# Optimization experiments

Hardware: AMD Instinct MI355X
Metric: run time of the kernel (lower is better)

The kernel has to match this reference:

```python
import jax, jax.numpy as jnp
import numpy as np

# Fully-refined octree (branching=2, initial_levels=7) == dense grid of resolution 128.
R = 128            # voxel grid resolution per axis (2**initial_levels)
SH_DIM = 9         # (sh_degree+1)**2, sh_degree=2
DATA_DIM = 28      # 3*SH_DIM + 1 (RGB SH coeffs + density)
N_STEPS = 128      # fixed ray-march step count (render_opt.n_steps)
BG = 1.0           # background brightness


def sh_basis(d):
    """Real SH basis up to degree 2 for unit directions d: [N,3] -> [N,9]."""
    x, y, z = d[:, 0], d[:, 1], d[:, 2]
    C0 = 0.28209479177387814
    C1 = 0.4886025119029199
    C2 = (1.0925484305920792, -1.0925484305920792, 0.31539156525252005,
          -1.0925484305920792, 0.5462742152960396)
    return jnp.stack([
        jnp.full_like(x, C0),
        -C1 * y, C1 * z, -C1 * x,
        C2[0] * x * y, C2[1] * y * z,
        C2[2] * (2.0 * z * z - x * x - y * y),
        C2[3] * x * z, C2[4] * (x * x - y * y),
    ], axis=-1)


def trilerp(grid, pts):
    """Trilinear interpolation. grid [R,R,R,C], pts [N,3] in grid coords."""
    Rg = grid.shape[0]
    p = jnp.clip(pts, 0.0, Rg - 1.0 - 1e-4)
    p0 = jnp.floor(p).astype(jnp.int32)
    w = p - p0.astype(p.dtype)
    out = jnp.zeros((pts.shape[0], grid.shape[-1]), grid.dtype)
    for dx in (0, 1):
        wx = w[:, 0] if dx else 1.0 - w[:, 0]
        for dy in (0, 1):
            wy = w[:, 1] if dy else 1.0 - w[:, 1]
            for dz in (0, 1):
                wz = w[:, 2] if dz else 1.0 - w[:, 2]
                out = out + (wx * wy * wz)[:, None] * grid[p0[:, 0] + dx, p0[:, 1] + dy, p0[:, 2] + dz]
    return out


def _render(grid, rays_o, rays_d, scaling, offset):
    dirs = rays_d / jnp.linalg.norm(rays_d, axis=-1, keepdims=True)   # world viewdirs
    o = rays_o * scaling + offset                                      # tree coords in [0,1]^3
    d = dirs * scaling
    delta_scale = 1.0 / jnp.linalg.norm(d, axis=-1)                    # world-space step scale
    invd = 1.0 / jnp.where(jnp.abs(d) > 1e-9, d, 1e-9)
    t1 = (0.0 - o) * invd
    t2 = (1.0 - o) * invd
    tmin = jnp.maximum(jnp.max(jnp.minimum(t1, t2), axis=-1), 0.0)
    tmax = jnp.min(jnp.maximum(t1, t2), axis=-1)
    valid = tmax > tmin
    dt = jnp.where(valid, (tmax - tmin) / N_STEPS, 0.0)                # per-ray step length
    basis = sh_basis(dirs)                                             # [N,9]
    N = rays_o.shape[0]

    def step(carry, i):
        T, rgb = carry
        t = tmin + (i.astype(grid.dtype) + 0.5) * dt
        pos = o + t[:, None] * d                                       # [N,3] in [0,1]^3
        vals = trilerp(grid, pos * R - 0.5)                            # [N,28]
        sigma = jnp.where(valid, jax.nn.relu(vals[:, -1]), 0.0)
        coeffs = vals[:, :3 * SH_DIM].reshape(N, 3, SH_DIM)
        c = jax.nn.sigmoid(jnp.einsum('nj,ncj->nc', basis, coeffs))    # [N,3]
        alpha = 1.0 - jnp.exp(-sigma * dt * delta_scale)
        rgb = rgb + (T * alpha)[:, None] * c
        T = T * (1.0 - alpha)
        return (T, rgb), None

    init = (jnp.ones((N,), grid.dtype), jnp.zeros((N, 3), grid.dtype))
    (T, rgb), _ = jax.lax.scan(step, init, jnp.arange(N_STEPS))
    return rgb + T[:, None] * BG


def setup_inputs() -> dict:
    key = jax.random.key(0)
    k1, k2, k3 = jax.random.split(key, 3)
    N = 32768
    rays_o = jax.random.uniform(k1, (N, 3), jnp.float32)               # inside unit cube
    rays_d = jax.random.normal(k2, (N, 3), jnp.float32)
    grid = jax.random.normal(k3, (R, R, R, DATA_DIM), jnp.float32) * 0.1  # octree leaf data
    scaling = jnp.ones((3,), jnp.float32)                              # 0.5/radius, radius=0.5
    offset = jnp.zeros((3,), jnp.float32)                              # 0.5 - center*scaling
    return {"rays_o": rays_o, "rays_d": rays_d, "grid": grid,
            "scaling": scaling, "offset": offset}


def reference(rays_o, rays_d, grid, scaling, offset):
    return _render(grid, rays_o, rays_d, scaling, offset)
```

## Files before the change

### kernel.cpp

```cpp
#include <hip/hip_runtime.h>
#include <math.h>

#define RGRID 128
#define NSTEPS 128
#define DATA_DIM 28

__device__ __forceinline__ float fast_rcp(float x) { return __builtin_amdgcn_rcpf(x); }

__global__ __launch_bounds__(256) void render_kernel(
    const float* __restrict__ rays_o,
    const float* __restrict__ rays_d,
    const float* __restrict__ grid,
    const float* __restrict__ scaling,
    const float* __restrict__ offset,
    float* __restrict__ out, int N)
{
    int tid = blockIdx.x * blockDim.x + threadIdx.x;
    int ray = tid >> 6;
    int lane = tid & 63;
    int s = lane >> 3;
    int c = lane & 7;
    if (ray >= N) return;

    float ox = rays_o[ray * 3 + 0], oy = rays_o[ray * 3 + 1], oz = rays_o[ray * 3 + 2];
    float rdx = rays_d[ray * 3 + 0], rdy = rays_d[ray * 3 + 1], rdz = rays_d[ray * 3 + 2];
    float sx = scaling[0], sy = scaling[1], sz = scaling[2];
    float fx = offset[0], fy = offset[1], fz = offset[2];

    float dn = rsqrtf(rdx * rdx + rdy * rdy + rdz * rdz);
    float dirx = rdx * dn, diry = rdy * dn, dirz = rdz * dn;

    float o0 = ox * sx + fx, o1 = oy * sy + fy, o2 = oz * sz + fz;
    float d0 = dirx * sx, d1 = diry * sy, d2 = dirz * sz;
    float delta_scale = rsqrtf(d0 * d0 + d1 * d1 + d2 * d2);

    float a0 = fabsf(d0) > 1e-9f ? d0 : 1e-9f;
    float a1 = fabsf(d1) > 1e-9f ? d1 : 1e-9f;
    float a2 = fabsf(d2) > 1e-9f ? d2 : 1e-9f;
    float i0 = 1.0f / a0, i1 = 1.0f / a1, i2 = 1.0f / a2;

    float t1x = (0.0f - o0) * i0, t2x = (1.0f - o0) * i0;
    float t1y = (0.0f - o1) * i1, t2y = (1.0f - o1) * i1;
    float t1z = (0.0f - o2) * i2, t2z = (1.0f - o2) * i2;
    float tmin = fmaxf(fmaxf(fminf(t1x, t2x), fminf(t1y, t2y)), fminf(t1z, t2z));
    tmin = fmaxf(tmin, 0.0f);
    float tmax = fminf(fminf(fmaxf(t1x, t2x), fmaxf(t1y, t2y)), fmaxf(t1z, t2z));
    bool valid = tmax > tmin;
    float dt = valid ? (tmax - tmin) * (1.0f / NSTEPS) : 0.0f;
    float sig_scale = dt * delta_scale;

    const float C0 = 0.28209479177387814f;
    const float C1 = 0.4886025119029199f;
    float b0 = C0;
    float b1 = -C1 * diry;
    float b2 = C1 * dirz;
    float b3 = -C1 * dirx;
    float b4 = 1.0925484305920792f * dirx * diry;
    float b5 = -1.0925484305920792f * diry * dirz;
    float b6 = 0.31539156525252005f * (2.0f * dirz * dirz - dirx * dirx - diry * diry);
    float b7 = -1.0925484305920792f * dirx * dirz;
    float b8 = 0.5462742152960396f * (dirx * dirx - diry * diry);

    int cdx = (c >> 2) & 1, cdy = (c >> 1) & 1, cdz = c & 1;
    int laneoff = (cdx << 14) + (cdy << 7) + cdz;
    float fsx = cdx ? 1.0f : -1.0f, fbx = cdx ? 0.0f : 1.0f;
    float fsy = cdy ? 1.0f : -1.0f, fby = cdy ? 0.0f : 1.0f;
    float fsz = cdz ? 1.0f : -1.0f, fbz = cdz ? 0.0f : 1.0f;

    float T = 1.0f, accr = 0.0f, accg = 0.0f, accb = 0.0f;
    float soff = (float)s + 0.5f;

    for (int it = 0; it < NSTEPS / 8; it++) {
        float t = tmin + ((float)(it * 8) + soff) * dt;
        float px = o0 + t * d0, py = o1 + t * d1, pz = o2 + t * d2;

        float gx = px * (float)RGRID - 0.5f;
        float gy = py * (float)RGRID - 0.5f;
        float gz = pz * (float)RGRID - 0.5f;
        gx = fminf(fmaxf(gx, 0.0f), 126.9999f);
        gy = fminf(fmaxf(gy, 0.0f), 126.9999f);
        gz = fminf(fmaxf(gz, 0.0f), 126.9999f);

        float flx = floorf(gx), fly = floorf(gy), flz = floorf(gz);
        int ix = (int)flx, iy = (int)fly, iz = (int)flz;
        float wx = gx - flx, wy = gy - fly, wz = gz - flz;

        float wgt = (fsx * wx + fbx) * (fsy * wy + fby) * (fsz * wz + fbz);

        int vox = (ix << 14) + (iy << 7) + iz + laneoff;
        const float4* gp = (const float4*)(grid + (size_t)vox * DATA_DIM);
        float4 v0 = gp[0], v1 = gp[1], v2 = gp[2], v3 = gp[3], v4 = gp[4], v5 = gp[5], v6 = gp[6];

        float vr = b0 * v0.x + b1 * v0.y + b2 * v0.z + b3 * v0.w
                 + b4 * v1.x + b5 * v1.y + b6 * v1.z + b7 * v1.w + b8 * v2.x;
        float vg = b0 * v2.y + b1 * v2.z + b2 * v2.w
                 + b3 * v3.x + b4 * v3.y + b5 * v3.z + b6 * v3.w
                 + b7 * v4.x + b8 * v4.y;
        float vb = b0 * v4.z + b1 * v4.w
                 + b2 * v5.x + b3 * v5.y + b4 * v5.z + b5 * v5.w
                 + b6 * v6.x + b7 * v6.y + b8 * v6.z;
        float vs = v6.w;

        vr *= wgt; vg *= wgt; vb *= wgt; vs *= wgt;

        #pragma unroll
        for (int m = 1; m < 8; m <<= 1) {
            vr += __shfl_xor(vr, m);
            vg += __shfl_xor(vg, m);
            vb += __shfl_xor(vb, m);
            vs += __shfl_xor(vs, m);
        }

        float sigma = valid ? fmaxf(vs, 0.0f) : 0.0f;
        float alpha = 1.0f - __expf(-sigma * sig_scale);
        float av = 1.0f - alpha;
        float br = alpha * fast_rcp(1.0f + __expf(-vr));
        float bg = alpha * fast_rcp(1.0f + __expf(-vg));
        float bb = alpha * fast_rcp(1.0f + __expf(-vb));

        #pragma unroll
        for (int d = 8; d < 64; d <<= 1) {
            float pa  = __shfl_up(av, d);
            float pbr = __shfl_up(br, d);
            float pbg = __shfl_up(bg, d);
            float pbb = __shfl_up(bb, d);
            if (lane >= d) {
                br = pbr + pa * br;
                bg = pbg + pa * bg;
                bb = pbb + pa * bb;
                av = pa * av;
            }
        }

        float ca  = __shfl(av, 63);
        float cbr = __shfl(br, 63);
        float cbg = __shfl(bg, 63);
        float cbb = __shfl(bb, 63);
        accr += T * cbr;
        accg += T * cbg;
        accb += T * cbb;
        T *= ca;
    }

    if (lane == 0) {
        out[ray * 3 + 0] = accr + T * 1.0f;
        out[ray * 3 + 1] = accg + T * 1.0f;
        out[ray * 3 + 2] = accb + T * 1.0f;
    }
}

extern "C" void kernel_launch(void* const* d_in, const int* in_sizes, int n_in,
                              void* d_out, int out_size, void* d_ws, size_t ws_size,
                              hipStream_t stream) {
    const float* rays_o  = (const float*)d_in[0];
    const float* rays_d  = (const float*)d_in[1];
    const float* grid    = (const float*)d_in[2];
    const float* scaling = (const float*)d_in[3];
    const float* offset  = (const float*)d_in[4];
    float* out = (float*)d_out;
    int N = in_sizes[0] / 3;

    int threads = 256;
    long long total = (long long)N * 64;
    int blocks = (int)((total + threads - 1) / threads);
    render_kernel<<<blocks, threads, 0, stream>>>(rays_o, rays_d, grid, scaling, offset, out, N);
}
```

Before: 489.4 us.

## Map one march step per lane with full trilinear gather per thread

Result: slower. 774.9 us (+58.3%).

```diff
diff --git a/kernel.cpp b/kernel.cpp
--- a/kernel.cpp
+++ b/kernel.cpp
@@ -18,8 +18,6 @@
     int tid = blockIdx.x * blockDim.x + threadIdx.x;
     int ray = tid >> 6;
     int lane = tid & 63;
-    int s = lane >> 3;
-    int c = lane & 7;
     if (ray >= N) return;
 
     float ox = rays_o[ray * 3 + 0], oy = rays_o[ray * 3 + 1], oz = rays_o[ray * 3 + 2];
@@ -61,17 +59,11 @@
     float b7 = -1.0925484305920792f * dirx * dirz;
     float b8 = 0.5462742152960396f * (dirx * dirx - diry * diry);
 
-    int cdx = (c >> 2) & 1, cdy = (c >> 1) & 1, cdz = c & 1;
-    int laneoff = (cdx << 14) + (cdy << 7) + cdz;
-    float fsx = cdx ? 1.0f : -1.0f, fbx = cdx ? 0.0f : 1.0f;
-    float fsy = cdy ? 1.0f : -1.0f, fby = cdy ? 0.0f : 1.0f;
-    float fsz = cdz ? 1.0f : -1.0f, fbz = cdz ? 0.0f : 1.0f;
+    float T = 1.0f, accr = 0.0f, accg = 0.0f, accb = 0.0f;
 
-    float T = 1.0f, accr = 0.0f, accg = 0.0f, accb = 0.0f;
-    float soff = (float)s + 0.5f;
-
-    for (int it = 0; it < NSTEPS / 8; it++) {
-        float t = tmin + ((float)(it * 8) + soff) * dt;
+    #pragma unroll
+    for (int half = 0; half < 2; half++) {
+        float t = tmin + ((float)(half * 64 + lane) + 0.5f) * dt;
         float px = o0 + t * d0, py = o1 + t * d1, pz = o2 + t * d2;
 
         float gx = px * (float)RGRID - 0.5f;
@@ -84,32 +76,61 @@
         float flx = floorf(gx), fly = floorf(gy), flz = floorf(gz);
         int ix = (int)flx, iy = (int)fly, iz = (int)flz;
         float wx = gx - flx, wy = gy - fly, wz = gz - flz;
+        float ux = 1.0f - wx, uy = 1.0f - wy, uz = 1.0f - wz;
 
-        float wgt = (fsx * wx + fbx) * (fsy * wy + fby) * (fsz * wz + fbz);
+        float wxy00 = ux * uy, wxy01 = ux * wy, wxy10 = wx * uy, wxy11 = wx * wy;
+        float w000 = wxy00 * uz, w001 = wxy00 * wz;
+        float w010 = wxy01 * uz, w011 = wxy01 * wz;
+        float w100 = wxy10 * uz, w101 = wxy10 * wz;
+        float w110 = wxy11 * uz, w111 = wxy11 * wz;
 
-        int vox = (ix << 14) + (iy << 7) + iz + laneoff;
-        const float4* gp = (const float4*)(grid + (size_t)vox * DATA_DIM);
-        float4 v0 = gp[0], v1 = gp[1], v2 = gp[2], v3 = gp[3], v4 = gp[4], v5 = gp[5], v6 = gp[6];
+        int voxbase = (ix * RGRID + iy) * RGRID + iz;
+        const float* base = grid + (size_t)voxbase * DATA_DIM;
 
-        float vr = b0 * v0.x + b1 * v0.y + b2 * v0.z + b3 * v0.w
-                 + b4 * v1.x + b5 * v1.y + b6 * v1.z + b7 * v1.w + b8 * v2.x;
-        float vg = b0 * v2.y + b1 * v2.z + b2 * v2.w
-                 + b3 * v3.x + b4 * v3.y + b5 * v3.z + b6 * v3.w
-                 + b7 * v4.x + b8 * v4.y;
-        float vb = b0 * v4.z + b1 * v4.w
-                 + b2 * v5.x + b3 * v5.y + b4 * v5.z + b5 * v5.w
-                 + b6 * v6.x + b7 * v6.y + b8 * v6.z;
-        float vs = v6.w;
+        float4 A0, A1, A2, A3, A4, A5, A6;
 
-        vr *= wgt; vg *= wgt; vb *= wgt; vs *= wgt;
+        {
+            const float4* gp = (const float4*)(base);
+            float4 u0 = gp[0], u1 = gp[1], u2 = gp[2], u3 = gp[3], u4 = gp[4], u5 = gp[5], u6 = gp[6];
+            float w = w000;
+            A0.x = w*u0.x; A0.y = w*u0.y; A0.z = w*u0.z; A0.w = w*u0.w;
+            A1.x = w*u1.x; A1.y = w*u1.y; A1.z = w*u1.z; A1.w = w*u1.w;
+            A2.x = w*u2.x; A2.y = w*u2.y; A2.z = w*u2.z; A2.w = w*u2.w;
+            A3.x = w*u3.x; A3.y = w*u3.y; A3.z = w*u3.z; A3.w = w*u3.w;
+            A4.x = w*u4.x; A4.y = w*u4.y; A4.z = w*u4.z; A4.w = w*u4.w;
+            A5.x = w*u5.x; A5.y = w*u5.y; A5.z = w*u5.z; A5.w = w*u5.w;
+            A6.x = w*u6.x; A6.y = w*u6.y; A6.z = w*u6.z; A6.w = w*u6.w;
+        }
+        #define ACC_CORNER(VOXOFF, W) { \
+            const float4* gp = (const float4*)(base + (VOXOFF) * DATA_DIM); \
+            float4 u0 = gp[0], u1 = gp[1], u2 = gp[2], u3 = gp[3], u4 = gp[4], u5 = gp[5], u6 = gp[6]; \
+            float w = (W); \
+            A0.x = fmaf(w, u0.x, A0.x); A0.y = fmaf(w, u0.y, A0.y); A0.z = fmaf(w, u0.z, A0.z); A0.w = fmaf(w, u0.w, A0.w); \
+            A1.x = fmaf(w, u1.x, A1.x); A1.y = fmaf(w, u1.y, A1.y); A1.z = fmaf(w, u1.z, A1.z); A1.w = fmaf(w, u1.w, A1.w); \
+            A2.x = fmaf(w, u2.x, A2.x); A2.y = fmaf(w, u2.y, A2.y); A2.z = fmaf(w, u2.z, A2.z); A2.w = fmaf(w, u2.w, A2.w); \
+            A3.x = fmaf(w, u3.x, A3.x); A3.y = fmaf(w, u3.y, A3.y); A3.z = fmaf(w, u3.z, A3.z); A3.w = fmaf(w, u3.w, A3.w); \
+            A4.x = fmaf(w, u4.x, A4.x); A4.y = fmaf(w, u4.y, A4.y); A4.z = fmaf(w, u4.z, A4.z); A4.w = fmaf(w, u4.w, A4.w); \
+            A5.x = fmaf(w, u5.x, A5.x); A5.y = fmaf(w, u5.y, A5.y); A5.z = fmaf(w, u5.z, A5.z); A5.w = fmaf(w, u5.w, A5.w); \
+            A6.x = fmaf(w, u6.x, A6.x); A6.y = fmaf(w, u6.y, A6.y); A6.z = fmaf(w, u6.z, A6.z); A6.w = fmaf(w, u6.w, A6.w); \
+        }
+        ACC_CORNER(1,             w001);
+        ACC_CORNER(RGRID,         w010);
+        ACC_CORNER(RGRID + 1,     w011);
+        ACC_CORNER(RGRID*RGRID,         w100);
+        ACC_CORNER(RGRID*RGRID + 1,     w101);
+        ACC_CORNER(RGRID*RGRID + RGRID,     w110);
+        ACC_CORNER(RGRID*RGRID + RGRID + 1, w111);
+        #undef ACC_CORNER
 
-        #pragma unroll
-        for (int m = 1; m < 8; m <<= 1) {
-            vr += __shfl_xor(vr, m);
-            vg += __shfl_xor(vg, m);
-            vb += __shfl_xor(vb, m);
-            vs += __shfl_xor(vs, m);
-        }
+        float vr = b0*A0.x + b1*A0.y + b2*A0.z + b3*A0.w
+                 + b4*A1.x + b5*A1.y + b6*A1.z + b7*A1.w + b8*A2.x;
+        float vg = b0*A2.y + b1*A2.z + b2*A2.w
+                 + b3*A3.x + b4*A3.y + b5*A3.z + b6*A3.w
+                 + b7*A4.x + b8*A4.y;
+        float vb = b0*A4.z + b1*A4.w
+                 + b2*A5.x + b3*A5.y + b4*A5.z + b5*A5.w
+                 + b6*A6.x + b7*A6.y + b8*A6.z;
+        float vs = A6.w;
 
         float sigma = valid ? fmaxf(vs, 0.0f) : 0.0f;
         float alpha = 1.0f - __expf(-sigma * sig_scale);
@@ -119,7 +140,7 @@
         float bb = alpha * fast_rcp(1.0f + __expf(-vb));
 
         #pragma unroll
-        for (int d = 8; d < 64; d <<= 1) {
+        for (int d = 1; d < 64; d <<= 1) {
             float pa  = __shfl_up(av, d);
             float pbr = __shfl_up(br, d);
             float pbg = __shfl_up(bg, d);
```

## Split render into setup, per-octet sampling, and per-ray compositing kernels

Applied to the files above, without the earlier changes.

Result: slower. 583.2 us (+19.2%).

```diff
diff --git a/kernel.cpp b/kernel.cpp
--- a/kernel.cpp
+++ b/kernel.cpp
@@ -6,6 +6,190 @@
 #define DATA_DIM 28
 
 __device__ __forceinline__ float fast_rcp(float x) { return __builtin_amdgcn_rcpf(x); }
+
+__global__ __launch_bounds__(256) void ray_setup_kernel(
+    const float* __restrict__ rays_o,
+    const float* __restrict__ rays_d,
+    const float* __restrict__ scaling,
+    const float* __restrict__ offset,
+    float* __restrict__ params, int N)
+{
+    int ray = blockIdx.x * blockDim.x + threadIdx.x;
+    if (ray >= N) return;
+
+    float ox = rays_o[ray * 3 + 0], oy = rays_o[ray * 3 + 1], oz = rays_o[ray * 3 + 2];
+    float rdx = rays_d[ray * 3 + 0], rdy = rays_d[ray * 3 + 1], rdz = rays_d[ray * 3 + 2];
+    float sx = scaling[0], sy = scaling[1], sz = scaling[2];
+    float fx = offset[0], fy = offset[1], fz = offset[2];
+
+    float dn = rsqrtf(rdx * rdx + rdy * rdy + rdz * rdz);
+    float dirx = rdx * dn, diry = rdy * dn, dirz = rdz * dn;
+
+    float o0 = ox * sx + fx, o1 = oy * sy + fy, o2 = oz * sz + fz;
+    float d0 = dirx * sx, d1 = diry * sy, d2 = dirz * sz;
+    float delta_scale = rsqrtf(d0 * d0 + d1 * d1 + d2 * d2);
+
+    float a0 = fabsf(d0) > 1e-9f ? d0 : 1e-9f;
+    float a1 = fabsf(d1) > 1e-9f ? d1 : 1e-9f;
+    float a2 = fabsf(d2) > 1e-9f ? d2 : 1e-9f;
+    float i0 = 1.0f / a0, i1 = 1.0f / a1, i2 = 1.0f / a2;
+
+    float t1x = (0.0f - o0) * i0, t2x = (1.0f - o0) * i0;
+    float t1y = (0.0f - o1) * i1, t2y = (1.0f - o1) * i1;
+    float t1z = (0.0f - o2) * i2, t2z = (1.0f - o2) * i2;
+    float tmin = fmaxf(fmaxf(fminf(t1x, t2x), fminf(t1y, t2y)), fminf(t1z, t2z));
+    tmin = fmaxf(tmin, 0.0f);
+    float tmax = fminf(fminf(fmaxf(t1x, t2x), fmaxf(t1y, t2y)), fmaxf(t1z, t2z));
+    bool valid = tmax > tmin;
+    float dt = valid ? (tmax - tmin) * (1.0f / NSTEPS) : 0.0f;
+    float sig_scale = dt * delta_scale;
+
+    const float C1 = 0.4886025119029199f;
+    float b1 = -C1 * diry;
+    float b2 = C1 * dirz;
+    float b3 = -C1 * dirx;
+    float b4 = 1.0925484305920792f * dirx * diry;
+    float b5 = -1.0925484305920792f * diry * dirz;
+    float b6 = 0.31539156525252005f * (2.0f * dirz * dirz - dirx * dirx - diry * diry);
+    float b7 = -1.0925484305920792f * dirx * dirz;
+    float b8 = 0.5462742152960396f * (dirx * dirx - diry * diry);
+
+    float4* P = (float4*)(params + (size_t)ray * 20);
+    P[0] = make_float4(o0, o1, o2, tmin);
+    P[1] = make_float4(d0, d1, d2, dt);
+    P[2] = make_float4(b1, b2, b3, b4);
+    P[3] = make_float4(b5, b6, b7, b8);
+    P[4] = make_float4(sig_scale, valid ? 1.0f : 0.0f, 0.0f, 0.0f);
+}
+
+__global__ __launch_bounds__(256) void sample_kernel(
+    const float* __restrict__ grid,
+    const float* __restrict__ params,
+    float* __restrict__ seg, int N)
+{
+    int tid = blockIdx.x * blockDim.x + threadIdx.x;
+    int unit = tid >> 6;
+    int lane = tid & 63;
+    int ray = unit >> 4;
+    int octet = unit & 15;
+    if (ray >= N) return;
+    int s = lane >> 3;
+    int c = lane & 7;
+
+    const float4* P = (const float4*)(params + (size_t)ray * 20);
+    float4 p0 = P[0], p1 = P[1], p2 = P[2], p3 = P[3], p4 = P[4];
+    float o0 = p0.x, o1 = p0.y, o2 = p0.z, tmin = p0.w;
+    float d0 = p1.x, d1 = p1.y, d2 = p1.z, dt = p1.w;
+    float b1 = p2.x, b2 = p2.y, b3 = p2.z, b4 = p2.w;
+    float b5 = p3.x, b6 = p3.y, b7 = p3.z, b8 = p3.w;
+    float sig_scale = p4.x;
+    bool valid = p4.y != 0.0f;
+    const float b0 = 0.28209479177387814f;
+
+    int cdx = (c >> 2) & 1, cdy = (c >> 1) & 1, cdz = c & 1;
+    int laneoff = (cdx << 14) + (cdy << 7) + cdz;
+    float fsx = cdx ? 1.0f : -1.0f, fbx = cdx ? 0.0f : 1.0f;
+    float fsy = cdy ? 1.0f : -1.0f, fby = cdy ? 0.0f : 1.0f;
+    float fsz = cdz ? 1.0f : -1.0f, fbz = cdz ? 0.0f : 1.0f;
+
+    int gstep = octet * 8 + s;
+    float t = tmin + ((float)gstep + 0.5f) * dt;
+    float px = o0 + t * d0, py = o1 + t * d1, pz = o2 + t * d2;
+
+    float gx = px * (float)RGRID - 0.5f;
+    float gy = py * (float)RGRID - 0.5f;
+    float gz = pz * (float)RGRID - 0.5f;
+    gx = fminf(fmaxf(gx, 0.0f), 126.9999f);
+    gy = fminf(fmaxf(gy, 0.0f), 126.9999f);
+    gz = fminf(fmaxf(gz, 0.0f), 126.9999f);
+
+    float flx = floorf(gx), fly = floorf(gy), flz = floorf(gz);
+    int ix = (int)flx, iy = (int)fly, iz = (int)flz;
+    float wx = gx - flx, wy = gy - fly, wz = gz - flz;
+
+    float wgt = (fsx * wx + fbx) * (fsy * wy + fby) * (fsz * wz + fbz);
+
+    int vox = (ix << 14) + (iy << 7) + iz + laneoff;
+    const float4* gp = (const float4*)(grid + (size_t)vox * DATA_DIM);
+    float4 v0 = gp[0], v1 = gp[1], v2 = gp[2], v3 = gp[3], v4 = gp[4], v5 = gp[5], v6 = gp[6];
+
+    float vr = b0 * v0.x + b1 * v0.y + b2 * v0.z + b3 * v0.w
+             + b4 * v1.x + b5 * v1.y + b6 * v1.z + b7 * v1.w + b8 * v2.x;
+    float vg = b0 * v2.y + b1 * v2.z + b2 * v2.w
+             + b3 * v3.x + b4 * v3.y + b5 * v3.z + b6 * v3.w
+             + b7 * v4.x + b8 * v4.y;
+    float vb = b0 * v4.z + b1 * v4.w
+             + b2 * v5.x + b3 * v5.y + b4 * v5.z + b5 * v5.w
+             + b6 * v6.x + b7 * v6.y + b8 * v6.z;
+    float vs = v6.w;
+
+    vr *= wgt; vg *= wgt; vb *= wgt; vs *= wgt;
+
+    #pragma unroll
+    for (int m = 1; m < 8; m <<= 1) {
+        vr += __shfl_xor(vr, m);
+        vg += __shfl_xor(vg, m);
+        vb += __shfl_xor(vb, m);
+        vs += __shfl_xor(vs, m);
+    }
+
+    float sigma = valid ? fmaxf(vs, 0.0f) : 0.0f;
+    float alpha = 1.0f - __expf(-sigma * sig_scale);
+    float av = 1.0f - alpha;
+    float br = alpha * fast_rcp(1.0f + __expf(-vr));
+    float bg = alpha * fast_rcp(1.0f + __expf(-vg));
+    float bb = alpha * fast_rcp(1.0f + __expf(-vb));
+
+    float v = (c == 0) ? av : ((c == 1) ? br : ((c == 2) ? bg : bb));
+    if (c < 4) seg[(size_t)ray * (NSTEPS * 4) + gstep * 4 + c] = v;
+}
+
+__global__ __launch_bounds__(256) void composite_kernel(
+    const float* __restrict__ seg,
+    float* __restrict__ out, int N)
+{
+    int tid = blockIdx.x * blockDim.x + threadIdx.x;
+    int ray = tid >> 6;
+    int lane = tid & 63;
+    if (ray >= N) return;
+
+    float T = 1.0f, accr = 0.0f, accg = 0.0f, accb = 0.0f;
+    const float4* sp = (const float4*)(seg + (size_t)ray * (NSTEPS * 4));
+
+    #pragma unroll
+    for (int half = 0; half < 2; half++) {
+        float4 v = sp[half * 64 + lane];
+        float av = v.x, br = v.y, bg = v.z, bb = v.w;
+
+        #pragma unroll
+        for (int d = 1; d < 64; d <<= 1) {
+            float pa  = __shfl_up(av, d);
+            float pbr = __shfl_up(br, d);
+            float pbg = __shfl_up(bg, d);
+            float pbb = __shfl_up(bb, d);
+            if (lane >= d) {
+                br = pbr + pa * br;
+                bg = pbg + pa * bg;
+                bb = pbb + pa * bb;
+                av = pa * av;
+            }
+        }
+        float ca  = __shfl(av, 63);
+        float cbr = __shfl(br, 63);
+        float cbg = __shfl(bg, 63);
+        float cbb = __shfl(bb, 63);
+        accr += T * cbr;
+        accg += T * cbg;
+        accb += T * cbb;
+        T *= ca;
+    }
+
+    if (lane == 0) {
+        out[ray * 3 + 0] = accr + T * 1.0f;
+        out[ray * 3 + 1] = accg + T * 1.0f;
+        out[ray * 3 + 2] = accb + T * 1.0f;
+    }
+}
 
 __global__ __launch_bounds__(256) void render_kernel(
     const float* __restrict__ rays_o,
@@ -160,8 +344,26 @@
     float* out = (float*)d_out;
     int N = in_sizes[0] / 3;
 
-    int threads = 256;
-    long long total = (long long)N * 64;
-    int blocks = (int)((total + threads - 1) / threads);
-    render_kernel<<<blocks, threads, 0, stream>>>(rays_o, rays_d, grid, scaling, offset, out, N);
-}
+    size_t seg_floats = (size_t)N * NSTEPS * 4;
+    size_t par_floats = (size_t)N * 20;
+    size_t need = (seg_floats + par_floats) * sizeof(float);
+
+    if (ws_size >= need) {
+        float* seg = (float*)d_ws;
+        float* params = seg + seg_floats;
+
+        ray_setup_kernel<<<(N + 255) / 256, 256, 0, stream>>>(
+            rays_o, rays_d, scaling, offset, params, N);
+
+        long long th1 = (long long)N * 16 * 64;
+        sample_kernel<<<(int)((th1 + 255) / 256), 256, 0, stream>>>(
+            grid, params, seg, N);
+
+        long long th2 = (long long)N * 64;
+        composite_kernel<<<(int)((th2 + 255) / 256), 256, 0, stream>>>(seg, out, N);
+    } else {
+        long long total = (long long)N * 64;
+        int blocks = (int)((total + 255) / 256);
+        render_kernel<<<blocks, 256, 0, stream>>>(rays_o, rays_d, grid, scaling, offset, out, N);
+    }
+}
```
